# Optimization experiments

Hardware: AMD Instinct MI355X
Metric: run time of the kernel (lower is better)

Reference implementation:

```python
import jax, jax.numpy as jnp
import numpy as np

EPS = 1e-8  # masked_log_softmax default eps


def setup_inputs() -> dict:
    key = jax.random.key(0)
    k1, k2, k3, k4, k5, k6 = jax.random.split(key, 6)
    B, T, S, L, D = 8, 128, 256, 256, 512  # batch, tgt_len, src_len(enc), src_length(proj), d_model
    decoder_hidden_state = jax.random.normal(k1, (B, T, D), dtype=jnp.float32)
    encoder_outputs = jax.random.normal(k2, (B, S, D), dtype=jnp.float32)
    mask = (jax.random.uniform(k3, (B, T, S)) > 0.3).astype(jnp.float32)
    W1 = jax.random.normal(k4, (L, D), dtype=jnp.float32) * 0.02  # Linear(d_model, src_length).weight
    W2 = jax.random.normal(k5, (L, D), dtype=jnp.float32) * 0.02
    vt = jax.random.normal(k6, (L,), dtype=jnp.float32) * 0.02   # Linear(src_length, 1).weight
    return {"decoder_hidden_state": decoder_hidden_state, "encoder_outputs": encoder_outputs,
            "mask": mask, "W1": W1, "W2": W2, "vt": vt}


def reference(decoder_hidden_state, encoder_outputs, mask, W1, W2, vt):
    # decoder_transform: (B, T, 1, L); encoder_transform: (B, 1, S, L)
    dec_t = jnp.einsum('btd,ld->btl', decoder_hidden_state, W1)[:, :, None, :]
    enc_t = jnp.einsum('bsd,ld->bsl', encoder_outputs, W2)[:, None, :, :]
    weights = jnp.tanh(dec_t + enc_t)                     # (B, T, S, L)
    scores = jnp.einsum('btsl,l->bts', weights, vt)       # vt reduction, squeeze(-1)
    logits = scores + jnp.log(mask + EPS)                 # masked log-softmax over src
    return jax.nn.log_softmax(logits, axis=-1)
```

## Files before the change

kernel.cpp:

```cpp
#include <hip/hip_runtime.h>

typedef __attribute__((ext_vector_type(8))) short short8;
typedef __attribute__((ext_vector_type(4))) float f32x4;

#define TANH_SCALE 2.8853900817779268f
#define LOG_EPS   -18.420680743952367f

static __device__ __forceinline__ unsigned short f2bf(float f) {
  unsigned u = __builtin_bit_cast(unsigned, f);
  u += 0x7FFFu + ((u >> 16) & 1u);
  return (unsigned short)(u >> 16);
}
static __device__ __forceinline__ float bf2f(unsigned short h) {
  unsigned u = (unsigned)h << 16;
  return __builtin_bit_cast(float, u);
}
static __device__ __forceinline__ short8 cvt8(float4 lo, float4 hi) {
  short8 r;
  r[0] = (short)f2bf(lo.x); r[1] = (short)f2bf(lo.y);
  r[2] = (short)f2bf(lo.z); r[3] = (short)f2bf(lo.w);
  r[4] = (short)f2bf(hi.x); r[5] = (short)f2bf(hi.y);
  r[6] = (short)f2bf(hi.z); r[7] = (short)f2bf(hi.w);
  return r;
}

__global__ __launch_bounds__(256) void gemm_proj_cvt(
    const float* __restrict__ W1, const float* __restrict__ W2,
    const float* __restrict__ dec, const float* __restrict__ enc,
    float* __restrict__ decPt, unsigned short* __restrict__ encPb) {
  const int K = 512;
  int idx = blockIdx.x;
  const float *A, *Bp;
  int N, mt, nt;
  bool is_dec = (idx < 128);
  size_t cbase = 0;
  if (is_dec) {
    A = W1; Bp = dec; N = 1024;
    mt = idx >> 5; nt = idx & 31;
  } else {
    int j = idx - 128, z = j >> 5, rem = j & 31;
    A = W2; Bp = enc + (size_t)z * 256 * K; N = 256;
    mt = rem >> 3; nt = rem & 7;
    cbase = (size_t)z * 256 * 256;
  }
  const int tid = threadIdx.x, wave = tid >> 6, lane = tid & 63;
  const int m0 = mt * 64 + wave * 16;
  const int n0 = nt * 32;
  const int l16 = lane & 15, quad = lane >> 4, kb = quad * 8;

  f32x4 acc0 = {0.f,0.f,0.f,0.f}, acc1 = {0.f,0.f,0.f,0.f};

  const float* ap  = A + (long)(m0 + l16) * K + kb;
  const float* bp0 = Bp + (long)(n0 + l16) * K + kb;
  const float* bp1 = bp0 + 16 * K;

  for (int ks = 0; ks < K; ks += 32) {
    float4 aL = *(const float4*)(ap + ks),  aH = *(const float4*)(ap + ks + 4);
    float4 b0L = *(const float4*)(bp0 + ks), b0H = *(const float4*)(bp0 + ks + 4);
    float4 b1L = *(const float4*)(bp1 + ks), b1H = *(const float4*)(bp1 + ks + 4);
    short8 a  = cvt8(aL, aH);
    short8 b0 = cvt8(b0L, b0H);
    short8 b1 = cvt8(b1L, b1H);
    acc0 = __builtin_amdgcn_mfma_f32_16x16x32_bf16(a, b0, acc0, 0, 0, 0);
    acc1 = __builtin_amdgcn_mfma_f32_16x16x32_bf16(a, b1, acc1, 0, 0, 0);
  }

  f32x4 accs[2] = {acc0, acc1};
  if (is_dec) {
#pragma unroll
    for (int j = 0; j < 2; ++j) {
      int n = n0 + j * 16 + l16;
#pragma unroll
      for (int r = 0; r < 4; ++r) {
        int m = m0 + quad * 4 + r;
        decPt[(long)m * N + n] = __builtin_amdgcn_exp2f(accs[j][r] * TANH_SCALE);
      }
    }
  } else {
#pragma unroll
    for (int j = 0; j < 2; ++j) {
      int n = n0 + j * 16 + l16;
#pragma unroll
      for (int r = 0; r < 4; ++r) {
        int m = m0 + quad * 4 + r;
        encPb[cbase + (long)m * N + n] =
            f2bf(__builtin_amdgcn_exp2f(accs[j][r] * TANH_SCALE));
      }
    }
  }
}

__global__ __launch_bounds__(1024) void fused_score_softmax(
    const float* __restrict__ decPt, const unsigned short* __restrict__ encPb,
    const float* __restrict__ mask, const float* __restrict__ vt,
    float* __restrict__ out) {
  const int T = 128, S = 256, L = 256;
  const int b = blockIdx.x >> 5;
  const int t0 = (blockIdx.x & 31) * 4;
  const int s = threadIdx.x & 255;
  const int q = threadIdx.x >> 8;
  const int l0 = q * (L / 4);

  const unsigned short* __restrict__ ep = encPb + (size_t)b * L * S + (size_t)l0 * S + s;
  const float* __restrict__ dp = decPt + (size_t)(b * T + t0) + (size_t)l0 * 1024;

  float acc0 = 0.f, acc1 = 0.f, acc2 = 0.f, acc3 = 0.f;
#pragma unroll 8
  for (int l = 0; l < L / 4; ++l) {
    float e = bf2f(ep[(size_t)l * S]);
    float4 P = *(const float4*)(dp + (size_t)l * 1024);
    float v = vt[l0 + l];
    float r0 = __builtin_amdgcn_rcpf(fmaf(P.x, e, 1.0f));
    float r1 = __builtin_amdgcn_rcpf(fmaf(P.y, e, 1.0f));
    float r2 = __builtin_amdgcn_rcpf(fmaf(P.z, e, 1.0f));
    float r3 = __builtin_amdgcn_rcpf(fmaf(P.w, e, 1.0f));
    acc0 = fmaf(v, r0, acc0);
    acc1 = fmaf(v, r1, acc1);
    acc2 = fmaf(v, r2, acc2);
    acc3 = fmaf(v, r3, acc3);
  }

  __shared__ float partial[4][4][256];
  partial[q][0][s] = acc0;
  partial[q][1][s] = acc1;
  partial[q][2][s] = acc2;
  partial[q][3][s] = acc3;
  __syncthreads();

  float lg = partial[0][q][s] + partial[1][q][s] + partial[2][q][s] + partial[3][q][s];

  const float LN2 = 0.6931471805599453f, L2E = 1.4426950408889634f;
  {
    float m = mask[(size_t)(b * T + t0 + q) * S + s];
    lg = fmaf(-2.0f, lg, (m != 0.0f) ? 0.0f : LOG_EPS);
  }

  __shared__ float redm[16], reds[16];
  const int wid = threadIdx.x >> 6, lane = threadIdx.x & 63;

  float w = lg;
#pragma unroll
  for (int off = 1; off < 64; off <<= 1) w = fmaxf(w, __shfl_xor(w, off));
  if (lane == 0) redm[wid] = w;
  __syncthreads();
  float bm = fmaxf(fmaxf(redm[q * 4 + 0], redm[q * 4 + 1]),
                   fmaxf(redm[q * 4 + 2], redm[q * 4 + 3]));

  float e = __builtin_amdgcn_exp2f((lg - bm) * L2E);
#pragma unroll
  for (int off = 1; off < 64; off <<= 1) e += __shfl_xor(e, off);
  if (lane == 0) reds[wid] = e;
  __syncthreads();
  float sum = reds[q * 4 + 0] + reds[q * 4 + 1] + reds[q * 4 + 2] + reds[q * 4 + 3];

  out[(size_t)(b * T + t0 + q) * S + s] = lg - bm - LN2 * __builtin_amdgcn_logf(sum);
}

extern "C" void kernel_launch(void* const* d_in, const int* in_sizes, int n_in,
                              void* d_out, int out_size, void* d_ws, size_t ws_size,
                              hipStream_t stream) {
  const int B = 8, T = 128;
  const float* dec = (const float*)d_in[0];
  const float* enc = (const float*)d_in[1];
  const float* mask = (const float*)d_in[2];
  const float* W1 = (const float*)d_in[3];
  const float* W2 = (const float*)d_in[4];
  const float* vt = (const float*)d_in[5];
  float* out = (float*)d_out;

  char* ws = (char*)d_ws;
  float* decPt = (float*)(ws);
  unsigned short* encPb = (unsigned short*)(ws + (1u << 20));

  gemm_proj_cvt<<<384, 256, 0, stream>>>(W1, W2, dec, enc, decPt, encPb);

  fused_score_softmax<<<B * T / 4, 1024, 0, stream>>>(decPt, encPb, mask, vt, out);
  (void)in_sizes; (void)n_in; (void)out_size; (void)ws_size;
}
```

Measured before the change: 106.4 us.

## Stage projection GEMM tiles through LDS with register prefetch

The projection GEMM previously had each wave load its own A and B fragments directly from global memory, so the B tile was fetched redundantly by all four waves. It now loads 64x128 and 32x128 chunks cooperatively with coalesced float4 reads, converts them to bf16 into padded LDS tiles, and prefetches the next K chunk into registers while the MFMAs run. The aim is less redundant global traffic and better coalescing in the first kernel. The cost is extra LDS use, two barriers per chunk and more registers per thread.

```diff
diff --git a/kernel.cpp b/kernel.cpp
--- a/kernel.cpp
+++ b/kernel.cpp
@@ -5,6 +5,8 @@
 
 #define TANH_SCALE 2.8853900817779268f
 #define LOG_EPS   -18.420680743952367f
+#define KC 128
+#define LDP (KC + 8)
 
 static __device__ __forceinline__ unsigned short f2bf(float f) {
   unsigned u = __builtin_bit_cast(unsigned, f);
@@ -14,14 +16,6 @@
 static __device__ __forceinline__ float bf2f(unsigned short h) {
   unsigned u = (unsigned)h << 16;
   return __builtin_bit_cast(float, u);
-}
-static __device__ __forceinline__ short8 cvt8(float4 lo, float4 hi) {
-  short8 r;
-  r[0] = (short)f2bf(lo.x); r[1] = (short)f2bf(lo.y);
-  r[2] = (short)f2bf(lo.z); r[3] = (short)f2bf(lo.w);
-  r[4] = (short)f2bf(hi.x); r[5] = (short)f2bf(hi.y);
-  r[6] = (short)f2bf(hi.z); r[7] = (short)f2bf(hi.w);
-  return r;
 }
 
 __global__ __launch_bounds__(256) void gemm_proj_cvt(
@@ -41,28 +35,67 @@
     int j = idx - 128, z = j >> 5, rem = j & 31;
     A = W2; Bp = enc + (size_t)z * 256 * K; N = 256;
     mt = rem >> 3; nt = rem & 7;
-    cbase = (size_t)z * 256 * 256;
+    cbase = (size_t)z * 65536;
   }
   const int tid = threadIdx.x, wave = tid >> 6, lane = tid & 63;
-  const int m0 = mt * 64 + wave * 16;
+  const int m0 = mt * 64;
   const int n0 = nt * 32;
   const int l16 = lane & 15, quad = lane >> 4, kb = quad * 8;
 
+  __shared__ unsigned short lA[64][LDP];
+  __shared__ unsigned short lB[32][LDP];
+
   f32x4 acc0 = {0.f,0.f,0.f,0.f}, acc1 = {0.f,0.f,0.f,0.f};
 
-  const float* ap  = A + (long)(m0 + l16) * K + kb;
-  const float* bp0 = Bp + (long)(n0 + l16) * K + kb;
-  const float* bp1 = bp0 + 16 * K;
-
-  for (int ks = 0; ks < K; ks += 32) {
-    float4 aL = *(const float4*)(ap + ks),  aH = *(const float4*)(ap + ks + 4);
-    float4 b0L = *(const float4*)(bp0 + ks), b0H = *(const float4*)(bp0 + ks + 4);
-    float4 b1L = *(const float4*)(bp1 + ks), b1H = *(const float4*)(bp1 + ks + 4);
-    short8 a  = cvt8(aL, aH);
-    short8 b0 = cvt8(b0L, b0H);
-    short8 b1 = cvt8(b1L, b1H);
-    acc0 = __builtin_amdgcn_mfma_f32_16x16x32_bf16(a, b0, acc0, 0, 0, 0);
-    acc1 = __builtin_amdgcn_mfma_f32_16x16x32_bf16(a, b1, acc1, 0, 0, 0);
+  float4 ra[8], rb[4];
+#pragma unroll
+  for (int i = 0; i < 8; ++i) {
+    int f = i * 256 + tid, row = f >> 5, c4 = f & 31;
+    ra[i] = *(const float4*)(A + (size_t)(m0 + row) * K + c4 * 4);
+  }
+#pragma unroll
+  for (int i = 0; i < 4; ++i) {
+    int f = i * 256 + tid, row = f >> 5, c4 = f & 31;
+    rb[i] = *(const float4*)(Bp + (size_t)(n0 + row) * K + c4 * 4);
+  }
+
+#pragma unroll
+  for (int kc = 0; kc < 4; ++kc) {
+#pragma unroll
+    for (int i = 0; i < 8; ++i) {
+      int f = i * 256 + tid, row = f >> 5, c4 = f & 31;
+      ushort4 o = { f2bf(ra[i].x), f2bf(ra[i].y), f2bf(ra[i].z), f2bf(ra[i].w) };
+      *(ushort4*)&lA[row][c4 * 4] = o;
+    }
+#pragma unroll
+    for (int i = 0; i < 4; ++i) {
+      int f = i * 256 + tid, row = f >> 5, c4 = f & 31;
+      ushort4 o = { f2bf(rb[i].x), f2bf(rb[i].y), f2bf(rb[i].z), f2bf(rb[i].w) };
+      *(ushort4*)&lB[row][c4 * 4] = o;
+    }
+    __syncthreads();
+    if (kc < 3) {
+      int k0n = (kc + 1) * KC;
+#pragma unroll
+      for (int i = 0; i < 8; ++i) {
+        int f = i * 256 + tid, row = f >> 5, c4 = f & 31;
+        ra[i] = *(const float4*)(A + (size_t)(m0 + row) * K + k0n + c4 * 4);
+      }
+#pragma unroll
+      for (int i = 0; i < 4; ++i) {
+        int f = i * 256 + tid, row = f >> 5, c4 = f & 31;
+        rb[i] = *(const float4*)(Bp + (size_t)(n0 + row) * K + k0n + c4 * 4);
+      }
+    }
+#pragma unroll
+    for (int ks = 0; ks < KC; ks += 32) {
+      short8 a  = *(const short8*)&lA[wave * 16 + l16][ks + kb];
+      short8 b0 = *(const short8*)&lB[l16][ks + kb];
+      short8 b1 = *(const short8*)&lB[16 + l16][ks + kb];
+      acc0 = __builtin_amdgcn_mfma_f32_16x16x32_bf16(a, b0, acc0, 0, 0, 0);
+      acc1 = __builtin_amdgcn_mfma_f32_16x16x32_bf16(a, b1, acc1, 0, 0, 0);
+    }
+    __syncthreads();
   }
 
   f32x4 accs[2] = {acc0, acc1};
@@ -72,7 +105,7 @@
       int n = n0 + j * 16 + l16;
 #pragma unroll
       for (int r = 0; r < 4; ++r) {
-        int m = m0 + quad * 4 + r;
+        int m = m0 + wave * 16 + quad * 4 + r;
         decPt[(long)m * N + n] = __builtin_amdgcn_exp2f(accs[j][r] * TANH_SCALE);
       }
     }
@@ -82,7 +115,7 @@
       int n = n0 + j * 16 + l16;
 #pragma unroll
       for (int r = 0; r < 4; ++r) {
-        int m = m0 + quad * 4 + r;
+        int m = m0 + wave * 16 + quad * 4 + r;
         encPb[cbase + (long)m * N + n] =
             f2bf(__builtin_amdgcn_exp2f(accs[j][r] * TANH_SCALE));
       }
```

Measured after the change: 90.90 us. 14.5% less time.
